# Kernel optimization log

Measured on AMD Instinct MI355X. Metric: run time of the kernel, lower is better.

## Reference

```python
import jax, jax.numpy as jnp
import numpy as np
from jax import lax

D, H_HEADS, DEPTH, E, HID, P, NCLS = 768, 12, 12, 4, 3072, 16, 1000

def _ln(x, w, b, eps=1e-5):
    m = x.mean(-1, keepdims=True)
    v = ((x - m) ** 2).mean(-1, keepdims=True)
    return (x - m) * lax.rsqrt(v + eps) * w + b

def setup_inputs() -> dict:
    key = jax.random.key(0)
    ks = jax.random.split(key, 16)
    s = 0.02
    inp = {
        'x': jax.random.normal(ks[0], (32, 3, 224, 224), jnp.float32),
        'conv_w': jax.random.normal(ks[1], (D, 3, P, P), jnp.float32) * s,
        'conv_b': jnp.zeros((D,), jnp.float32),
        'cls_token': jnp.zeros((1, 1, D), jnp.float32),
        'pos_embed': jax.random.normal(ks[2], (1, 197, D), jnp.float32) * s,
        'ln1_w': jnp.ones((DEPTH, D), jnp.float32),
        'ln1_b': jnp.zeros((DEPTH, D), jnp.float32),
        'qkv_w': jax.random.normal(ks[3], (DEPTH, 3 * D, D), jnp.float32) * s,
        'qkv_b': jnp.zeros((DEPTH, 3 * D), jnp.float32),
        'out_w': jax.random.normal(ks[4], (DEPTH, D, D), jnp.float32) * s,
        'out_b': jnp.zeros((DEPTH, D), jnp.float32),
        'ln2_w': jnp.ones((DEPTH, D), jnp.float32),
        'ln2_b': jnp.zeros((DEPTH, D), jnp.float32),
        'gate_w': jax.random.normal(ks[5], (DEPTH, E, D), jnp.float32) * s,
        'gate_b': jnp.zeros((DEPTH, E), jnp.float32),
        'e1_w': jax.random.normal(ks[6], (DEPTH, E, HID, D), jnp.float32) * s,
        'e1_b': jnp.zeros((DEPTH, E, HID), jnp.float32),
        'e2_w': jax.random.normal(ks[7], (DEPTH, E, D, HID), jnp.float32) * s,
        'e2_b': jnp.zeros((DEPTH, E, D), jnp.float32),
        'fnorm_w': jnp.ones((D,), jnp.float32),
        'fnorm_b': jnp.zeros((D,), jnp.float32),
        'head_w': jax.random.normal(ks[8], (NCLS, D), jnp.float32) * s,
        'head_b': jnp.zeros((NCLS,), jnp.float32),
    }
    return inp

def reference(x, conv_w, conv_b, cls_token, pos_embed, ln1_w, ln1_b, qkv_w, qkv_b,
              out_w, out_b, ln2_w, ln2_b, gate_w, gate_b, e1_w, e1_b, e2_w, e2_b,
              fnorm_w, fnorm_b, head_w, head_b):
    B = x.shape[0]
    # patch embedding: conv stride=patch, then flatten -> [B, N, D]
    x = lax.conv_general_dilated(x, conv_w, (P, P), 'VALID',
                                 dimension_numbers=('NCHW', 'OIHW', 'NCHW'))
    x = x + conv_b[None, :, None, None]
    x = x.reshape(B, D, -1).transpose(0, 2, 1)
    x = jnp.concatenate([jnp.broadcast_to(cls_token, (B, 1, D)), x], axis=1)
    x = x + pos_embed
    N = x.shape[1]
    hd = D // H_HEADS
    for i in range(DEPTH):
        # --- attention ---
        h = x
        y = _ln(x, ln1_w[i], ln1_b[i])
        qkv = y @ qkv_w[i].T + qkv_b[i]                      # [B,N,3D]
        q, k, v = jnp.split(qkv, 3, axis=-1)
        q = q.reshape(B, N, H_HEADS, hd).transpose(0, 2, 1, 3) / jnp.sqrt(hd).astype(x.dtype)
        k = k.reshape(B, N, H_HEADS, hd).transpose(0, 2, 1, 3)
        v = v.reshape(B, N, H_HEADS, hd).transpose(0, 2, 1, 3)
        attn = jax.nn.softmax(jnp.einsum('bhqd,bhkd->bhqk', q, k), axis=-1)
        ctx = jnp.einsum('bhqk,bhkd->bhqd', attn, v).transpose(0, 2, 1, 3).reshape(B, N, D)
        x = h + (ctx @ out_w[i].T + out_b[i])
        # --- MoE MLP (dense: all experts computed then masked, top_k=1) ---
        h = x
        y = _ln(x, ln2_w[i], ln2_b[i])
        gate = y @ gate_w[i].T + gate_b[i]                   # [B,N,E]
        topk_scores, topk_idx = lax.top_k(gate, 1)           # [B,N,1]
        score = jax.nn.softmax(topk_scores, axis=-1)[..., 0]  # [B,N] (==1 for k=1)
        h1 = jax.nn.gelu(jnp.einsum('bnd,ehd->benh', y, e1_w[i])
                         + e1_b[i][None, :, None, :], approximate=False)  # [B,E,N,HID]
        oe = jnp.einsum('benh,edh->bend', h1, e2_w[i]) + e2_b[i][None, :, None, :]
        mask = jax.nn.one_hot(topk_idx[..., 0], E, dtype=y.dtype)  # [B,N,E]
        moe = jnp.einsum('bne,bend->bnd', mask * score[..., None], oe)
        x = h + moe
    x = _ln(x, fnorm_w, fnorm_b)
    cls = x[:, 0]
    return cls @ head_w.T + head_b
```

## Files before the change

kernel.cpp:

```cpp
#include <hip/hip_runtime.h>
#include <hip/hip_bf16.h>
#include <math.h>

#define D_MODEL 768
#define SEQ     197
#define BATCH   32
#define NTOK    (BATCH*SEQ)
#define NHEAD   12
#define HDIM    64
#define NEXP    4
#define HID_N   3072
#define DEPTH_N 12

typedef __attribute__((ext_vector_type(4))) float f32x4;
typedef __attribute__((ext_vector_type(8))) short bf16x8;
typedef __attribute__((ext_vector_type(2))) unsigned int u32x2;

static __device__ __forceinline__ unsigned short f2bf(float f){
  unsigned int u = __builtin_bit_cast(unsigned int, f);
  u += 0x7FFFu + ((u >> 16) & 1u);
  return (unsigned short)(u >> 16);
}
static __device__ __forceinline__ void split_bf(float x, unsigned short& h, unsigned short& l){
  h = f2bf(x);
  float hf = __builtin_bit_cast(float, (unsigned)h << 16);
  l = f2bf(x - hf);
}

static __device__ __forceinline__ float wred_sum(float v){
  #pragma unroll
  for (int off = 32; off; off >>= 1) v += __shfl_down(v, off);
  return v;
}

template<int MODE>
__global__ __launch_bounds__(256, 2) void gemm_bf16x3(
    const float* __restrict__ A, const float* __restrict__ W,
    const float* __restrict__ bias, const float* __restrict__ resid,
    float* __restrict__ C, const float* __restrict__ pos,
    const int* __restrict__ toks, const int* __restrict__ cnts,
    const int* __restrict__ offs, int M, int N, int K)
{
  const int tid = threadIdx.x;
  int cnt = M, base = 0;
  if (MODE == 2 || MODE == 3){
    cnt  = cnts[blockIdx.z];
    base = offs[blockIdx.z];
    if ((int)blockIdx.x * 128 >= cnt) return;
    W    += (size_t)blockIdx.z * N * K;
    bias += (size_t)blockIdx.z * N;
  }
  const int m0 = blockIdx.x * 128, n0 = blockIdx.y * 128;

  __shared__ __align__(16) unsigned short Ah[128][40];
  __shared__ __align__(16) unsigned short Al[128][40];
  __shared__ __align__(16) unsigned short Wh[128][40];
  __shared__ __align__(16) unsigned short Wl[128][40];

  const int srow = tid >> 3;
  const int kc   = (tid & 7) * 4;
  const float* pA[4];
  const float* pW[4];
  size_t pbase4[4];
  #pragma unroll
  for (int p = 0; p < 4; p++){
    int r  = p * 32 + srow;
    int gm = m0 + r;
    if (MODE == 0 || MODE == 1) pA[p] = (gm < M)   ? A + (size_t)gm * K : nullptr;
    if (MODE == 2)              pA[p] = (gm < cnt) ? A + (size_t)toks[base + gm] * K : nullptr;
    if (MODE == 3)              pA[p] = (gm < cnt) ? A + (size_t)(base + gm) * K : nullptr;
    if (MODE == 4){
      int b_ = gm / 196, pp = gm - b_ * 196;
      int py = pp / 14,  px = pp - py * 14;
      pbase4[p] = (size_t)b_ * 150528 + (size_t)py * 3584 + (size_t)px * 16;
      pA[p] = A;
    }
    pW[p] = W + (size_t)(n0 + r) * K;
  }

  const int NT = K >> 5;
  const int lane = tid & 63, wid = tid >> 6;
  const int wr = wid >> 1, wc = wid & 1;
  const int lr = lane & 15, lq = lane >> 4;

  f32x4 acc[4][4] = {};

  auto LOAD = [&](int kt, f32x4* vA, f32x4* vW){
    const int k = kt * 32 + kc;
    #pragma unroll
    for (int p = 0; p < 4; p++){
      if (MODE == 4){
        size_t off = pbase4[p] + (size_t)(k >> 8) * 50176
                   + (size_t)((k >> 4) & 15) * 224 + (size_t)(k & 15);
        vA[p] = *reinterpret_cast<const f32x4*>(A + off);
      } else {
        vA[p] = pA[p] ? *reinterpret_cast<const f32x4*>(pA[p] + k)
                      : f32x4{0.f, 0.f, 0.f, 0.f};
      }
      vW[p] = *reinterpret_cast<const f32x4*>(pW[p] + k);
    }
  };
  auto STORE = [&](const f32x4* vA, const f32x4* vW){
    #pragma unroll
    for (int p = 0; p < 4; p++){
      int r = p * 32 + srow;
      unsigned short h0,h1,h2,h3,l0,l1,l2,l3;
      split_bf(vA[p][0], h0, l0); split_bf(vA[p][1], h1, l1);
      split_bf(vA[p][2], h2, l2); split_bf(vA[p][3], h3, l3);
      u32x2 hp, lp;
      hp[0] = (unsigned)h0 | ((unsigned)h1 << 16); hp[1] = (unsigned)h2 | ((unsigned)h3 << 16);
      lp[0] = (unsigned)l0 | ((unsigned)l1 << 16); lp[1] = (unsigned)l2 | ((unsigned)l3 << 16);
      *reinterpret_cast<u32x2*>(&Ah[r][kc]) = hp;
      *reinterpret_cast<u32x2*>(&Al[r][kc]) = lp;
      split_bf(vW[p][0], h0, l0); split_bf(vW[p][1], h1, l1);
      split_bf(vW[p][2], h2, l2); split_bf(vW[p][3], h3, l3);
      hp[0] = (unsigned)h0 | ((unsigned)h1 << 16); hp[1] = (unsigned)h2 | ((unsigned)h3 << 16);
      lp[0] = (unsigned)l0 | ((unsigned)l1 << 16); lp[1] = (unsigned)l2 | ((unsigned)l3 << 16);
      *reinterpret_cast<u32x2*>(&Wh[r][kc]) = hp;
      *reinterpret_cast<u32x2*>(&Wl[r][kc]) = lp;
    }
  };

  {
    f32x4 cA[4], cW[4];
    LOAD(0, cA, cW);
    STORE(cA, cW);
  }
  __syncthreads();

  for (int t = 0; t < NT; t++){
    f32x4 nA[4], nW[4];
    if (t + 1 < NT) LOAD(t + 1, nA, nW);
    bf16x8 afh[4], afl[4], bfh[4], bfl[4];
    #pragma unroll
    for (int mi = 0; mi < 4; mi++){
      afh[mi] = *reinterpret_cast<const bf16x8*>(&Ah[wr*64 + mi*16 + lr][lq*8]);
      afl[mi] = *reinterpret_cast<const bf16x8*>(&Al[wr*64 + mi*16 + lr][lq*8]);
    }
    #pragma unroll
    for (int nj = 0; nj < 4; nj++){
      bfh[nj] = *reinterpret_cast<const bf16x8*>(&Wh[wc*64 + nj*16 + lr][lq*8]);
      bfl[nj] = *reinterpret_cast<const bf16x8*>(&Wl[wc*64 + nj*16 + lr][lq*8]);
    }
    #pragma unroll
    for (int mi = 0; mi < 4; mi++)
      #pragma unroll
      for (int nj = 0; nj < 4; nj++){
        acc[mi][nj] = __builtin_amdgcn_mfma_f32_16x16x32_bf16(afh[mi], bfh[nj], acc[mi][nj], 0, 0, 0);
        acc[mi][nj] = __builtin_amdgcn_mfma_f32_16x16x32_bf16(afh[mi], bfl[nj], acc[mi][nj], 0, 0, 0);
        acc[mi][nj] = __builtin_amdgcn_mfma_f32_16x16x32_bf16(afl[mi], bfh[nj], acc[mi][nj], 0, 0, 0);
      }
    __syncthreads();
    if (t + 1 < NT){
      STORE(nA, nW);
      __syncthreads();
    }
  }

  #pragma unroll
  for (int nj = 0; nj < 4; nj++){
    const int ncol = n0 + wc*64 + nj*16 + lr;
    const float bv = bias[ncol];
    #pragma unroll
    for (int mi = 0; mi < 4; mi++){
      const int mb = m0 + wr*64 + mi*16 + lq*4;
      #pragma unroll
      for (int j = 0; j < 4; j++){
        const int m = mb + j;
        float v = acc[mi][nj][j] + bv;
        if (MODE == 0){
          if (m < M) C[(size_t)m * N + ncol] = v;
        }
        if (MODE == 1){
          if (m < M) C[(size_t)m * N + ncol] = v + resid[(size_t)m * N + ncol];
        }
        if (MODE == 2){
          if (m < cnt){
            v = 0.5f * v * (1.f + erff(v * 0.70710678118f));
            C[(size_t)(base + m) * N + ncol] = v;
          }
        }
        if (MODE == 3){
          if (m < cnt){
            int tok = toks[base + m];
            C[(size_t)tok * N + ncol] += v;
          }
        }
        if (MODE == 4){
          int b_ = m / 196, pp = m - b_ * 196;
          C[((size_t)b_ * 197 + 1 + pp) * D_MODEL + ncol] =
              v + pos[(size_t)(1 + pp) * D_MODEL + ncol];
        }
      }
    }
  }
}

__global__ __launch_bounds__(256) void cls_init(const float* __restrict__ cls_tk,
                                                const float* __restrict__ pos,
                                                float* __restrict__ xt){
  const int b = blockIdx.x, tid = threadIdx.x;
  for (int d = tid; d < D_MODEL; d += 256)
    xt[((size_t)b*SEQ)*D_MODEL + d] = cls_tk[d] + pos[d];
}

__global__ __launch_bounds__(256) void ln_kernel(const float* __restrict__ x, size_t xstride,
                                                 const float* __restrict__ w,
                                                 const float* __restrict__ b,
                                                 float* __restrict__ y, size_t ystride){
  const int t = blockIdx.x;
  const int tid = threadIdx.x;
  const float* row = x + (size_t)t*xstride;
  float v0 = row[tid], v1 = row[tid+256], v2 = row[tid+512];
  __shared__ float red[4];
  float s = wred_sum(v0+v1+v2);
  if ((tid & 63) == 0) red[tid>>6] = s;
  __syncthreads();
  const float mean = (red[0]+red[1]+red[2]+red[3]) * (1.f/768.f);
  const float d0 = v0-mean, d1 = v1-mean, d2 = v2-mean;
  __syncthreads();
  float q = wred_sum(d0*d0 + d1*d1 + d2*d2);
  if ((tid & 63) == 0) red[tid>>6] = q;
  __syncthreads();
  const float var = (red[0]+red[1]+red[2]+red[3]) * (1.f/768.f);
  const float inv = rsqrtf(var + 1e-5f);
  float* yr = y + (size_t)t*ystride;
  yr[tid]     = d0*inv*w[tid]     + b[tid];
  yr[tid+256] = d1*inv*w[tid+256] + b[tid+256];
  yr[tid+512] = d2*inv*w[tid+512] + b[tid+512];
}

__global__ __launch_bounds__(256, 3) void attn_f32(const float* __restrict__ qkv,
                                                   float* __restrict__ ctx){
  const int qt = blockIdx.x, h = blockIdx.y, b = blockIdx.z;
  const int tid = threadIdx.x;
  const int tx = tid & 15, ty = tid >> 4;
  __shared__ float Qs[64][65];
  __shared__ float KPs[64][65];
  __shared__ float Vs[64][65];
  const size_t rs = 3*D_MODEL;
  const float* base = qkv + (size_t)b*SEQ*rs + (size_t)h*HDIM;

  #pragma unroll
  for (int it = 0; it < 16; it++){
    int idx = tid + it*256;
    int r = idx >> 6, c = idx & 63;
    int gq = qt*64 + r;
    float v = (gq < SEQ) ? base[(size_t)gq*rs + c] : 0.f;
    Qs[r][c] = v * 0.125f;
  }
  float m_run[4], l_run[4], o[4][4];
  #pragma unroll
  for (int i = 0; i < 4; i++){
    m_run[i] = -3.0e38f; l_run[i] = 0.f;
    #pragma unroll
    for (int j = 0; j < 4; j++) o[i][j] = 0.f;
  }
  __syncthreads();

  for (int kt = 0; kt < 4; kt++){
    #pragma unroll
    for (int it = 0; it < 16; it++){
      int idx = tid + it*256;
      int r = idx >> 6, c = idx & 63;
      int gk = kt*64 + r;
      float kv = (gk < SEQ) ? base[(size_t)gk*rs + D_MODEL   + c] : 0.f;
      float vv = (gk < SEQ) ? base[(size_t)gk*rs + 2*D_MODEL + c] : 0.f;
      KPs[r][c] = kv;
      Vs[r][c]  = vv;
    }
    __syncthreads();
    float s[4][4] = {};
    for (int d = 0; d < 64; d++){
      float qv[4], kv2[4];
      #pragma unroll
      for (int i = 0; i < 4; i++) qv[i]  = Qs[ty*4+i][d];
      #pragma unroll
      for (int j = 0; j < 4; j++) kv2[j] = KPs[tx*4+j][d];
      #pragma unroll
      for (int i = 0; i < 4; i++)
        #pragma unroll
        for (int j = 0; j < 4; j++) s[i][j] += qv[i]*kv2[j];
    }
    #pragma unroll
    for (int j = 0; j < 4; j++){
      if (kt*64 + tx*4 + j >= SEQ){
        #pragma unroll
        for (int i = 0; i < 4; i++) s[i][j] = -3.0e38f;
      }
    }
    float scale[4];
    #pragma unroll
    for (int i = 0; i < 4; i++){
      float mt = fmaxf(fmaxf(s[i][0], s[i][1]), fmaxf(s[i][2], s[i][3]));
      #pragma unroll
      for (int msk = 1; msk <= 8; msk <<= 1) mt = fmaxf(mt, __shfl_xor(mt, msk));
      float mnew = fmaxf(m_run[i], mt);
      scale[i] = __expf(m_run[i] - mnew);
      float ls = 0.f;
      #pragma unroll
      for (int j = 0; j < 4; j++){ s[i][j] = __expf(s[i][j] - mnew); ls += s[i][j]; }
      #pragma unroll
      for (int msk = 1; msk <= 8; msk <<= 1) ls += __shfl_xor(ls, msk);
      l_run[i] = l_run[i]*scale[i] + ls;
      m_run[i] = mnew;
    }
    __syncthreads();
    #pragma unroll
    for (int i = 0; i < 4; i++)
      #pragma unroll
      for (int j = 0; j < 4; j++) KPs[ty*4+i][tx*4+j] = s[i][j];
    __syncthreads();
    #pragma unroll
    for (int i = 0; i < 4; i++)
      #pragma unroll
      for (int j = 0; j < 4; j++) o[i][j] *= scale[i];
    for (int k = 0; k < 64; k++){
      float pv[4], vv[4];
      #pragma unroll
      for (int i = 0; i < 4; i++) pv[i] = KPs[ty*4+i][k];
      #pragma unroll
      for (int j = 0; j < 4; j++) vv[j] = Vs[k][tx*4+j];
      #pragma unroll
      for (int i = 0; i < 4; i++)
        #pragma unroll
        for (int j = 0; j < 4; j++) o[i][j] += pv[i]*vv[j];
    }
    __syncthreads();
  }
  #pragma unroll
  for (int i = 0; i < 4; i++){
    int q = qt*64 + ty*4 + i;
    if (q < SEQ){
      float inv = 1.f / l_run[i];
      #pragma unroll
      for (int j = 0; j < 4; j++)
        ctx[((size_t)(b*SEQ + q))*D_MODEL + h*HDIM + tx*4 + j] = o[i][j]*inv;
    }
  }
}

__global__ __launch_bounds__(256) void gate_kernel(const float* __restrict__ y,
                                                   const float* __restrict__ gw,
                                                   const float* __restrict__ gb,
                                                   int* __restrict__ eidx){
  const int t = blockIdx.x;
  const int tid = threadIdx.x;
  const int e = tid >> 6, lane = tid & 63;
  const float* row = y + (size_t)t*D_MODEL;
  const float* wrow = gw + (size_t)e*D_MODEL;
  float acc = 0.f;
  for (int k = lane; k < D_MODEL; k += 64) acc += row[k]*wrow[k];
  acc = wred_sum(acc);
  __shared__ float sc[NEXP];
  if (lane == 0) sc[e] = acc + gb[e];
  __syncthreads();
  if (tid == 0){
    int best = 0; float bv = sc[0];
    #pragma unroll
    for (int k = 1; k < NEXP; k++) if (sc[k] > bv){ bv = sc[k]; best = k; }
    eidx[t] = best;
  }
}

__global__ void zero_counts(int* c){ if (threadIdx.x < 3*NEXP) c[threadIdx.x] = 0; }

__global__ __launch_bounds__(256) void count_kernel(const int* __restrict__ eidx, int* counts){
  int i = blockIdx.x*256 + threadIdx.x;
  if (i < NTOK) atomicAdd(&counts[eidx[i]], 1);
}

__global__ void offsets_kernel(const int* counts, int* offs, int* cursor){
  if (threadIdx.x == 0){
    int o = 0;
    for (int e = 0; e < NEXP; e++){ offs[e] = o; cursor[e] = o; o += counts[e]; }
  }
}

__global__ __launch_bounds__(256) void scatter_kernel(const int* __restrict__ eidx,
                                                      int* cursor, int* __restrict__ toks){
  int i = blockIdx.x*256 + threadIdx.x;
  if (i < NTOK){ int pos = atomicAdd(&cursor[eidx[i]], 1); toks[pos] = i; }
}

__global__ __launch_bounds__(256) void gemm_f32(const float* __restrict__ A,
                                                const float* __restrict__ W,
                                                const float* __restrict__ bias,
                                                const float* __restrict__ resid,
                                                float* __restrict__ C,
                                                int M, int N, int K){
  const int m0 = blockIdx.x*64, bn = blockIdx.y*64;
  const int tid = threadIdx.x;
  const int tx = tid & 15, ty = tid >> 4;
  __shared__ float As[16][65];
  __shared__ float Ws[16][65];
  float acc[4][4] = {};
  for (int k0 = 0; k0 < K; k0 += 16){
    #pragma unroll
    for (int i = 0; i < 4; i++){
      int idx = tid + i*256;
      int k = idx & 15, m = idx >> 4;
      As[k][m] = (m0+m < M) ? A[(size_t)(m0+m)*K + k0 + k] : 0.f;
      Ws[k][m] = (bn+m < N) ? W[(size_t)(bn+m)*K + k0 + k] : 0.f;
    }
    __syncthreads();
    #pragma unroll
    for (int kk = 0; kk < 16; kk++){
      float a0 = As[kk][ty*4+0], a1 = As[kk][ty*4+1], a2 = As[kk][ty*4+2], a3 = As[kk][ty*4+3];
      float w0 = Ws[kk][tx*4+0], w1 = Ws[kk][tx*4+1], w2 = Ws[kk][tx*4+2], w3 = Ws[kk][tx*4+3];
      acc[0][0] += a0*w0; acc[0][1] += a0*w1; acc[0][2] += a0*w2; acc[0][3] += a0*w3;
      acc[1][0] += a1*w0; acc[1][1] += a1*w1; acc[1][2] += a1*w2; acc[1][3] += a1*w3;
      acc[2][0] += a2*w0; acc[2][1] += a2*w1; acc[2][2] += a2*w2; acc[2][3] += a2*w3;
      acc[3][0] += a3*w0; acc[3][1] += a3*w1; acc[3][2] += a3*w2; acc[3][3] += a3*w3;
    }
    __syncthreads();
  }
  #pragma unroll
  for (int i = 0; i < 4; i++){
    int m = m0 + ty*4 + i;
    if (m >= M) continue;
    #pragma unroll
    for (int j = 0; j < 4; j++){
      int n = bn + tx*4 + j;
      if (n >= N) continue;
      float v = acc[i][j];
      if (bias)  v += bias[n];
      if (resid) v += resid[(size_t)m*N + n];
      C[(size_t)m*N + n] = v;
    }
  }
}

extern "C" void kernel_launch(void* const* d_in, const int* in_sizes, int n_in,
                              void* d_out, int out_size, void* d_ws, size_t ws_size,
                              hipStream_t stream){
  const float* x      = (const float*)d_in[0];
  const float* conv_w = (const float*)d_in[1];
  const float* conv_b = (const float*)d_in[2];
  const float* cls_tk = (const float*)d_in[3];
  const float* pos    = (const float*)d_in[4];
  const float* ln1w   = (const float*)d_in[5];
  const float* ln1b   = (const float*)d_in[6];
  const float* qkvw   = (const float*)d_in[7];
  const float* qkvb   = (const float*)d_in[8];
  const float* outw   = (const float*)d_in[9];
  const float* outb   = (const float*)d_in[10];
  const float* ln2w   = (const float*)d_in[11];
  const float* ln2b   = (const float*)d_in[12];
  const float* gatew  = (const float*)d_in[13];
  const float* gateb  = (const float*)d_in[14];
  const float* e1w    = (const float*)d_in[15];
  const float* e1b    = (const float*)d_in[16];
  const float* e2w    = (const float*)d_in[17];
  const float* e2b    = (const float*)d_in[18];
  const float* fnw    = (const float*)d_in[19];
  const float* fnb    = (const float*)d_in[20];
  const float* headw  = (const float*)d_in[21];
  const float* headb  = (const float*)d_in[22];
  float* out = (float*)d_out;

  float* ws    = (float*)d_ws;
  float* xt    = ws;
  float* y     = xt  + (size_t)NTOK*D_MODEL;
  float* qkv   = y   + (size_t)NTOK*D_MODEL;
  float* ctx   = qkv + (size_t)NTOK*3*D_MODEL;
  float* h1    = ctx + (size_t)NTOK*D_MODEL;
  float* clsln = h1  + (size_t)NTOK*HID_N;
  int*   eidx   = (int*)(clsln + (size_t)BATCH*D_MODEL);
  int*   toks   = eidx + NTOK;
  int*   counts = toks + NTOK;
  int*   offs   = counts + NEXP;
  int*   cursor = offs + NEXP;

  dim3 b256(256);

  gemm_bf16x3<4><<<dim3(49, 6), b256, 0, stream>>>(x, conv_w, conv_b, nullptr, xt,
      pos, nullptr, nullptr, nullptr, 6272, D_MODEL, 768);
  cls_init<<<dim3(BATCH), b256, 0, stream>>>(cls_tk, pos, xt);

  for (int i = 0; i < DEPTH_N; i++){
    ln_kernel<<<dim3(NTOK), b256, 0, stream>>>(xt, D_MODEL,
        ln1w + (size_t)i*D_MODEL, ln1b + (size_t)i*D_MODEL, y, D_MODEL);
    gemm_bf16x3<0><<<dim3(50, 18), b256, 0, stream>>>(y,
        qkvw + (size_t)i*3*D_MODEL*D_MODEL, qkvb + (size_t)i*3*D_MODEL,
        nullptr, qkv, nullptr, nullptr, nullptr, nullptr, NTOK, 3*D_MODEL, D_MODEL);
    attn_f32<<<dim3(4, NHEAD, BATCH), b256, 0, stream>>>(qkv, ctx);
    gemm_bf16x3<1><<<dim3(50, 6), b256, 0, stream>>>(ctx,
        outw + (size_t)i*D_MODEL*D_MODEL, outb + (size_t)i*D_MODEL,
        xt, xt, nullptr, nullptr, nullptr, nullptr, NTOK, D_MODEL, D_MODEL);
    ln_kernel<<<dim3(NTOK), b256, 0, stream>>>(xt, D_MODEL,
        ln2w + (size_t)i*D_MODEL, ln2b + (size_t)i*D_MODEL, y, D_MODEL);
    gate_kernel<<<dim3(NTOK), b256, 0, stream>>>(y,
        gatew + (size_t)i*NEXP*D_MODEL, gateb + (size_t)i*NEXP, eidx);
    zero_counts<<<1, 64, 0, stream>>>(counts);
    count_kernel<<<dim3((NTOK+255)/256), b256, 0, stream>>>(eidx, counts);
    offsets_kernel<<<1, 64, 0, stream>>>(counts, offs, cursor);
    scatter_kernel<<<dim3((NTOK+255)/256), b256, 0, stream>>>(eidx, cursor, toks);
    gemm_bf16x3<2><<<dim3(50, HID_N/128, NEXP), b256, 0, stream>>>(y,
        e1w + (size_t)i*NEXP*HID_N*D_MODEL, e1b + (size_t)i*NEXP*HID_N,
        nullptr, h1, nullptr, toks, counts, offs, NTOK, HID_N, D_MODEL);
    gemm_bf16x3<3><<<dim3(50, D_MODEL/128, NEXP), b256, 0, stream>>>(h1,
        e2w + (size_t)i*NEXP*D_MODEL*HID_N, e2b + (size_t)i*NEXP*D_MODEL,
        nullptr, xt, nullptr, toks, counts, offs, NTOK, D_MODEL, HID_N);
  }

  ln_kernel<<<dim3(BATCH), b256, 0, stream>>>(xt, (size_t)SEQ*D_MODEL, fnw, fnb, clsln, D_MODEL);
  gemm_f32<<<dim3(1, 16), b256, 0, stream>>>(clsln, headw, headb, nullptr, out, BATCH, 1000, D_MODEL);
}
```

Measured before the change: 11.47 ms.

## Flatten GEMM grids with XCD-aware tile remap and compact MoE expert tile list

Turns the GEMM launches into 1D grids and remaps block IDs so consecutive logical tiles land on the same XCD, sharing the same weight column block in its L2. For the MoE expert GEMMs, offsets_kernel now builds a compact list of (expert, m0) tiles. This replaces the 50x4 padded grid with 53 tile slots, so fewer blocks launch only to exit early. The cost is integer div/mod per block plus a serial tile-list build in a single thread.

```diff
diff --git a/kernel.cpp b/kernel.cpp
--- a/kernel.cpp
+++ b/kernel.cpp
@@ -33,24 +33,40 @@
   return v;
 }
 
+static __device__ __forceinline__ int xcd_map(int orig, int nwg){
+  int q = nwg >> 3, r = nwg & 7;
+  int xcd = orig & 7, idx = orig >> 3;
+  return (xcd < r ? xcd*(q+1) : r*(q+1) + (xcd-r)*q) + idx;
+}
+
 template<int MODE>
 __global__ __launch_bounds__(256, 2) void gemm_bf16x3(
     const float* __restrict__ A, const float* __restrict__ W,
     const float* __restrict__ bias, const float* __restrict__ resid,
     float* __restrict__ C, const float* __restrict__ pos,
     const int* __restrict__ toks, const int* __restrict__ cnts,
-    const int* __restrict__ offs, int M, int N, int K)
+    const int* __restrict__ offs, const int* __restrict__ tiles,
+    int M, int N, int K)
 {
   const int tid = threadIdx.x;
-  int cnt = M, base = 0;
+  const int NB = N >> 7;
+  const int nm = gridDim.x / NB;
+  const int lg = xcd_map(blockIdx.x, gridDim.x);
+  const int mt = lg % nm, nb = lg / nm;
+
+  int cnt = M, base = 0, m0;
   if (MODE == 2 || MODE == 3){
-    cnt  = cnts[blockIdx.z];
-    base = offs[blockIdx.z];
-    if ((int)blockIdx.x * 128 >= cnt) return;
-    W    += (size_t)blockIdx.z * N * K;
-    bias += (size_t)blockIdx.z * N;
-  }
-  const int m0 = blockIdx.x * 128, n0 = blockIdx.y * 128;
+    if (mt >= tiles[0]) return;
+    const int e = tiles[1 + 2*mt];
+    m0 = tiles[2 + 2*mt];
+    cnt  = cnts[e];
+    base = offs[e];
+    W    += (size_t)e * N * K;
+    bias += (size_t)e * N;
+  } else {
+    m0 = mt * 128;
+  }
+  const int n0 = nb * 128;
 
   __shared__ __align__(16) unsigned short Ah[128][40];
   __shared__ __align__(16) unsigned short Al[128][40];
@@ -370,10 +386,17 @@
   if (i < NTOK) atomicAdd(&counts[eidx[i]], 1);
 }
 
-__global__ void offsets_kernel(const int* counts, int* offs, int* cursor){
+__global__ void offsets_kernel(const int* counts, int* offs, int* cursor, int* tiles){
   if (threadIdx.x == 0){
-    int o = 0;
-    for (int e = 0; e < NEXP; e++){ offs[e] = o; cursor[e] = o; o += counts[e]; }
+    int o = 0, n = 0;
+    for (int e = 0; e < NEXP; e++){
+      offs[e] = o; cursor[e] = o;
+      for (int m0 = 0; m0 < counts[e]; m0 += 128){
+        tiles[1+2*n] = e; tiles[2+2*n] = m0; n++;
+      }
+      o += counts[e];
+    }
+    tiles[0] = n;
   }
 }
 
@@ -471,37 +494,38 @@
   int*   counts = toks + NTOK;
   int*   offs   = counts + NEXP;
   int*   cursor = offs + NEXP;
+  int*   tiles  = cursor + NEXP;
 
   dim3 b256(256);
 
-  gemm_bf16x3<4><<<dim3(49, 6), b256, 0, stream>>>(x, conv_w, conv_b, nullptr, xt,
-      pos, nullptr, nullptr, nullptr, 6272, D_MODEL, 768);
+  gemm_bf16x3<4><<<dim3(49*6), b256, 0, stream>>>(x, conv_w, conv_b, nullptr, xt,
+      pos, nullptr, nullptr, nullptr, nullptr, 6272, D_MODEL, 768);
   cls_init<<<dim3(BATCH), b256, 0, stream>>>(cls_tk, pos, xt);
 
   for (int i = 0; i < DEPTH_N; i++){
     ln_kernel<<<dim3(NTOK), b256, 0, stream>>>(xt, D_MODEL,
         ln1w + (size_t)i*D_MODEL, ln1b + (size_t)i*D_MODEL, y, D_MODEL);
-    gemm_bf16x3<0><<<dim3(50, 18), b256, 0, stream>>>(y,
+    gemm_bf16x3<0><<<dim3(50*18), b256, 0, stream>>>(y,
         qkvw + (size_t)i*3*D_MODEL*D_MODEL, qkvb + (size_t)i*3*D_MODEL,
-        nullptr, qkv, nullptr, nullptr, nullptr, nullptr, NTOK, 3*D_MODEL, D_MODEL);
+        nullptr, qkv, nullptr, nullptr, nullptr, nullptr, nullptr, NTOK, 3*D_MODEL, D_MODEL);
     attn_f32<<<dim3(4, NHEAD, BATCH), b256, 0, stream>>>(qkv, ctx);
-    gemm_bf16x3<1><<<dim3(50, 6), b256, 0, stream>>>(ctx,
+    gemm_bf16x3<1><<<dim3(50*6), b256, 0, stream>>>(ctx,
         outw + (size_t)i*D_MODEL*D_MODEL, outb + (size_t)i*D_MODEL,
-        xt, xt, nullptr, nullptr, nullptr, nullptr, NTOK, D_MODEL, D_MODEL);
+        xt, xt, nullptr, nullptr, nullptr, nullptr, nullptr, NTOK, D_MODEL, D_MODEL);
     ln_kernel<<<dim3(NTOK), b256, 0, stream>>>(xt, D_MODEL,
         ln2w + (size_t)i*D_MODEL, ln2b + (size_t)i*D_MODEL, y, D_MODEL);
     gate_kernel<<<dim3(NTOK), b256, 0, stream>>>(y,
         gatew + (size_t)i*NEXP*D_MODEL, gateb + (size_t)i*NEXP, eidx);
     zero_counts<<<1, 64, 0, stream>>>(counts);
     count_kernel<<<dim3((NTOK+255)/256), b256, 0, stream>>>(eidx, counts);
-    offsets_kernel<<<1, 64, 0, stream>>>(counts, offs, cursor);
+    offsets_kernel<<<1, 64, 0, stream>>>(counts, offs, cursor, tiles);
     scatter_kernel<<<dim3((NTOK+255)/256), b256, 0, stream>>>(eidx, cursor, toks);
-    gemm_bf16x3<2><<<dim3(50, HID_N/128, NEXP), b256, 0, stream>>>(y,
+    gemm_bf16x3<2><<<dim3(53*(HID_N/128)), b256, 0, stream>>>(y,
         e1w + (size_t)i*NEXP*HID_N*D_MODEL, e1b + (size_t)i*NEXP*HID_N,
-        nullptr, h1, nullptr, toks, counts, offs, NTOK, HID_N, D_MODEL);
-    gemm_bf16x3<3><<<dim3(50, D_MODEL/128, NEXP), b256, 0, stream>>>(h1,
+        nullptr, h1, nullptr, toks, counts, offs, tiles, NTOK, HID_N, D_MODEL);
+    gemm_bf16x3<3><<<dim3(53*(D_MODEL/128)), b256, 0, stream>>>(h1,
         e2w + (size_t)i*NEXP*D_MODEL*HID_N, e2b + (size_t)i*NEXP*D_MODEL,
-        nullptr, xt, nullptr, toks, counts, offs, NTOK, D_MODEL, HID_N);
+        nullptr, xt, nullptr, toks, counts, offs, tiles, NTOK, D_MODEL, HID_N);
   }
 
   ln_kernel<<<dim3(BATCH), b256, 0, stream>>>(xt, (size_t)SEQ*D_MODEL, fnw, fnb, clsln, D_MODEL);
```

After: 11.02 ms. -3.9%, faster.
